# Optimization experiments

Measured on AMD Instinct MI355X. Metric: run time of the kernel, lower is better.

Reference implementation:

```python
import jax, jax.numpy as jnp
import numpy as np

B, T = 32, 64
C, H, W = 1, 32, 32
A, E, D, S, HID = 2, 64, 128, 32, 128
K, STRIDE, PAD = 4, 2, 1
FEAT = 64 * 4 * 4  # conv stack output: 64 channels at 4x4


def _lin(x, w, b):
    return x @ w.T + b


def _conv(x, w, b):
    y = jax.lax.conv_general_dilated(x, w, (STRIDE, STRIDE), [(PAD, PAD)] * 2,
                                     dimension_numbers=('NCHW', 'OIHW', 'NCHW'))
    return y + b[None, :, None, None]


def _deconv(x, w, b):
    # torch ConvTranspose2d(w: (in_c,out_c,k,k), stride=2, pad=1) as dilated conv
    w_ = jnp.flip(w, (2, 3)).transpose(1, 0, 2, 3)
    p = K - 1 - PAD
    y = jax.lax.conv_general_dilated(x, w_, (1, 1), [(p, p)] * 2,
                                     lhs_dilation=(STRIDE, STRIDE),
                                     dimension_numbers=('NCHW', 'OIHW', 'NCHW'))
    return y + b[None, :, None, None]


def _mlp(x, w1, b1, w2, b2, w3, b3):
    h = jax.nn.elu(_lin(x, w1, b1))
    h = jax.nn.elu(_lin(h, w2, b2))
    out = _lin(h, w3, b3)
    return out[..., :S], jnp.clip(out[..., S:], -5.0, 2.0)


def _gru(x, h, wih, whh, bih, bhh):
    # torch nn.GRUCell semantics
    gi = x @ wih.T + bih
    gh = h @ whh.T + bhh
    ir, iz, inn = jnp.split(gi, 3, -1)
    hr, hz, hn = jnp.split(gh, 3, -1)
    r = jax.nn.sigmoid(ir + hr)
    u = jax.nn.sigmoid(iz + hz)
    n = jnp.tanh(inn + r * hn)
    return (1.0 - u) * n + u * h


def setup_inputs():
    keys = iter(jax.random.split(jax.random.key(0), 64))

    def p(shape, fan):
        return jax.random.normal(next(keys), shape, jnp.float32) / np.sqrt(fan)

    return dict(
        obs=jax.random.normal(next(keys), (B, T, C, H, W), jnp.float32),
        actions=jax.random.normal(next(keys), (B, T, A), jnp.float32),
        noise=jax.random.normal(next(keys), (T, B, S), jnp.float32),
        enc_w1=p((32, C, K, K), C * K * K), enc_b1=jnp.zeros(32),
        enc_w2=p((64, 32, K, K), 32 * K * K), enc_b2=jnp.zeros(64),
        enc_w3=p((64, 64, K, K), 64 * K * K), enc_b3=jnp.zeros(64),
        enc_pw=p((E, FEAT), FEAT), enc_pb=jnp.zeros(E),
        dec_pw=p((FEAT, D + S), D + S), dec_pb=jnp.zeros(FEAT),
        dec_w1=p((64, 64, K, K), 64 * K * K), dec_b1=jnp.zeros(64),
        dec_w2=p((64, 32, K, K), 64 * K * K), dec_b2=jnp.zeros(32),
        dec_w3=p((32, C, K, K), 32 * K * K), dec_b3=jnp.zeros(C),
        gru_wih=p((3 * D, S + A), D), gru_whh=p((3 * D, D), D),
        gru_bih=jnp.zeros(3 * D), gru_bhh=jnp.zeros(3 * D),
        pri_w1=p((HID, D + A), D + A), pri_b1=jnp.zeros(HID),
        pri_w2=p((HID, HID), HID), pri_b2=jnp.zeros(HID),
        pri_w3=p((2 * S, HID), HID), pri_b3=jnp.zeros(2 * S),
        pos_w1=p((HID, D + E), D + E), pos_b1=jnp.zeros(HID),
        pos_w2=p((HID, HID), HID), pos_b2=jnp.zeros(HID),
        pos_w3=p((2 * S, HID), HID), pos_b3=jnp.zeros(2 * S),
    )


def reference(obs, actions, noise, enc_w1, enc_b1, enc_w2, enc_b2, enc_w3, enc_b3,
              enc_pw, enc_pb, dec_pw, dec_pb, dec_w1, dec_b1, dec_w2, dec_b2,
              dec_w3, dec_b3, gru_wih, gru_whh, gru_bih, gru_bhh,
              pri_w1, pri_b1, pri_w2, pri_b2, pri_w3, pri_b3,
              pos_w1, pos_b1, pos_w2, pos_b2, pos_w3, pos_b3):
    Bq, Tq = obs.shape[:2]
    # --- CNN encoder over all frames at once ---
    x = obs.reshape(Bq * Tq, C, H, W)
    x = jax.nn.relu(_conv(x, enc_w1, enc_b1))
    x = jax.nn.relu(_conv(x, enc_w2, enc_b2))
    x = jax.nn.relu(_conv(x, enc_w3, enc_b3))
    embed = _lin(x.reshape(Bq * Tq, -1), enc_pw, enc_pb).reshape(Bq, Tq, E)

    # --- sequential RSSM core (use_posterior=True path) ---
    def step(h, inp):
        a, e_t, eps = inp
        pm, pls = _mlp(jnp.concatenate([h, e_t], -1),
                       pos_w1, pos_b1, pos_w2, pos_b2, pos_w3, pos_b3)
        z = pm + jnp.exp(pls) * eps
        prm, prls = _mlp(jnp.concatenate([h, a], -1),
                         pri_w1, pri_b1, pri_w2, pri_b2, pri_w3, pri_b3)
        h_new = _gru(jnp.concatenate([z, a], -1), h, gru_wih, gru_whh, gru_bih, gru_bhh)
        return h_new, (z, prm, prls, pm, pls, h)  # h = pre-update (used for decode)

    h0 = jnp.zeros((Bq, D), obs.dtype)
    h_final, (zs, prm, prls, pm, pls, hs) = jax.lax.scan(
        step, h0, (actions.swapaxes(0, 1), embed.swapaxes(0, 1), noise))

    # --- batched decode of all (h_t, z_t); same math as per-step decode ---
    hz = jnp.concatenate([hs, zs], -1).reshape(Tq * Bq, D + S)
    y = _lin(hz, dec_pw, dec_pb).reshape(Tq * Bq, 64, 4, 4)
    y = jax.nn.relu(_deconv(y, dec_w1, dec_b1))
    y = jax.nn.relu(_deconv(y, dec_w2, dec_b2))
    y = jax.nn.sigmoid(_deconv(y, dec_w3, dec_b3))
    recons = y.reshape(Tq, Bq, C, H, W).swapaxes(0, 1)

    tb = lambda t: t.swapaxes(0, 1)  # (T,B,.) -> (B,T,.)
    return (recons, tb(zs), tb(prm), tb(prls), tb(pm), tb(pls), h_final)
```

## Files before the change

kernel.cpp:

```cpp
#include <hip/hip_runtime.h>
#include <math.h>

#define NB 32
#define NT 64
#define NF 2048

#define OUT_ZS    2097152
#define OUT_PRM   (OUT_ZS + 65536)
#define OUT_PRLS  (OUT_PRM + 65536)
#define OUT_PM    (OUT_PRLS + 65536)
#define OUT_PLS   (OUT_PM + 65536)
#define OUT_HF    (OUT_PLS + 65536)

#define WS_HS    27394048
#define WS_ENCT  27656192
#define WS_DECT  27721728
#define WS_WP1H  27885568
#define WS_WP2   27893760
#define WS_WP3   27901952
#define WS_WWHH  27906048
#define WS_WIHZ  27930624
#define WS_QW1T  27936768
#define WS_QW2T  27953408
#define WS_QW3T  27969792
#define WS_PW1T  27977984
#define WS_WIHT  28002560
#define WS_WC2   16777216
#define WS_WC3   (WS_WC2 + 16384)
#define WS_WD1   (WS_WC3 + 32768)
#define WS_WD2   (WS_WD1 + 32768)
#define WS_POSL1E 25165824
#define WS_GIA    (WS_POSL1E + 262144)

typedef __attribute__((ext_vector_type(8))) short short8;
typedef __attribute__((ext_vector_type(4))) float floatx4;
typedef _Float16 __attribute__((ext_vector_type(2))) half2v;
union U4S8 { uint4 u; short8 s; };
__device__ __forceinline__ short8 u2s(uint4 u) { U4S8 x; x.u = u; return x.s; }
__device__ __forceinline__ float eluf(float a) { return (a > 0.f) ? a : expm1f(a); }
__device__ __forceinline__ float sigm(float a) { return 1.f / (1.f + expf(-a)); }
__device__ __forceinline__ unsigned short f2bf(float f) {
  unsigned int u = __float_as_uint(f);
  u += 0x7fffu + ((u >> 16) & 1u);
  return (unsigned short)(u >> 16);
}
__device__ __forceinline__ unsigned short f2h(float f) {
  _Float16 h = (_Float16)f;
  return __builtin_bit_cast(unsigned short, h);
}
union UH2 { unsigned int u; half2v h; };
__device__ __forceinline__ half2v u2h(unsigned int u) { UH2 x; x.u = u; return x.h; }

__device__ __forceinline__ float fdot2w(half2v a, half2v b, float c) {
#if __has_builtin(__builtin_amdgcn_fdot2)
  return __builtin_amdgcn_fdot2(a, b, c, false);
#else
  return fmaf((float)a[0], (float)b[0], fmaf((float)a[1], (float)b[1], c));
#endif
}

union U4H2 { uint4 u; half2v h[4]; };
__device__ __forceinline__ void dot8h(uint4 w, uint4 x,
                                      float& a0, float& a1, float& a2, float& a3) {
  U4H2 W; W.u = w;
  U4H2 X; X.u = x;
  a0 = fdot2w(W.h[0], X.h[0], a0);
  a1 = fdot2w(W.h[1], X.h[1], a1);
  a2 = fdot2w(W.h[2], X.h[2], a2);
  a3 = fdot2w(W.h[3], X.h[3], a3);
}

struct PP { const float* src; void* dst; int n; int mode; int A; int B; };
struct PPAll { PP m[16]; };

__global__ __launch_bounds__(256) void k_prep(PPAll a) {
  PP p = a.m[blockIdx.y];
  for (int i = blockIdx.x * 256 + threadIdx.x; i < p.n; i += gridDim.x * 256) {
    if (p.mode == 10) {
      const int r = i / p.B, c = i - r * p.B;
      ((float*)p.dst)[c * p.A + r] = p.src[i];
    } else {
      float v;
      if (p.mode == 0) v = p.src[i];
      else if (p.mode == 1) v = p.src[(i >> 7) * 192 + (i & 127)];
      else if (p.mode == 2) v = p.src[(i >> 5) * 34 + (i & 31)];
      else if (p.mode == 5) {
        const int kq = i >> 12, o = (i >> 2) & 1023, kl = (i >> 1) & 1, h = i & 1;
        v = p.src[o * 160 + kq * 4 + kl * 2 + h];
      } else {
        const int ab = p.A * p.B;
        const int t = i / ab, rem = i - t * ab;
        const int oc = rem / p.B, ic = rem - oc * p.B;
        v = (p.mode == 3) ? p.src[(oc * p.B + ic) * 16 + t]
                          : p.src[(ic * p.A + oc) * 16 + t];
      }
      ((unsigned short*)p.dst)[i] = (p.mode <= 2 || p.mode == 5) ? f2h(v) : f2bf(v);
    }
  }
}

__global__ __launch_bounds__(256, 2) void k_enc(
    const float* __restrict__ obs, const float* __restrict__ act,
    const float* __restrict__ w1, const float* __restrict__ b1,
    const unsigned short* __restrict__ wc2, const float* __restrict__ b2,
    const unsigned short* __restrict__ wc3, const float* __restrict__ b3,
    const float* __restrict__ encT, const float* __restrict__ encb,
    const float* __restrict__ pw1T, const float* __restrict__ pb1,
    const float* __restrict__ wihT, const float* __restrict__ bih,
    float* __restrict__ posl1e, float* __restrict__ gia) {
  const int f = blockIdx.x, tid = threadIdx.x;
  const int w = tid >> 6, l = tid & 63, q = l >> 4, n = l & 15;
  __shared__ float sIn1[32 * 33];
  __shared__ float sW1[512];
  __shared__ float sB1[32];
  __shared__ __align__(16) unsigned short sIn2[18 * 18 * 40];
  __shared__ __align__(16) unsigned short sIn3[10 * 10 * 72];
  __shared__ __align__(16) float sXe[1024];
  __shared__ float sP[256];
  __shared__ float sE[64];
  __shared__ float sA2[2];

  {
    const float* in = obs + (size_t)f * 1024;
    for (int i = tid; i < 1024; i += 256) sIn1[(i >> 5) * 33 + (i & 31)] = in[i];
    for (int i = tid; i < 512; i += 256) sW1[i] = w1[i];
    if (tid < 32) sB1[tid] = b1[tid];
    if (tid < 2) sA2[tid] = act[(size_t)f * 2 + tid];
    unsigned int* z2 = (unsigned int*)sIn2;
    for (int i = tid; i < 18 * 18 * 40 / 2; i += 256) z2[i] = 0u;
    unsigned int* z3 = (unsigned int*)sIn3;
    for (int i = tid; i < 10 * 10 * 72 / 2; i += 256) z3[i] = 0u;
  }
  __syncthreads();
  for (int r = tid; r < 512; r += 256) {
    const int oc = r >> 4, oy = r & 15;
    float acc[16];
    const float bv = sB1[oc];
#pragma unroll
    for (int j = 0; j < 16; j++) acc[j] = bv;
#pragma unroll
    for (int ky = 0; ky < 4; ky++) {
      const int iy = 2 * oy + ky - 1;
      if (iy < 0 || iy >= 32) continue;
#pragma unroll
      for (int kx = 0; kx < 4; kx++) {
        const float wv = sW1[oc * 16 + ky * 4 + kx];
#pragma unroll
        for (int j = 0; j < 16; j++) {
          const int ix = 2 * j + kx - 1;
          if (ix >= 0 && ix < 32) acc[j] += wv * sIn1[iy * 33 + ix];
        }
      }
    }
#pragma unroll
    for (int j = 0; j < 16; j++)
      sIn2[((oy + 1) * 18 + (j + 1)) * 40 + oc] = f2bf(fmaxf(acc[j], 0.f));
  }
  __syncthreads();
  {
    int base[4];
#pragma unroll
    for (int nt = 0; nt < 4; nt++) {
      const int px = nt * 16 + n, oy = px >> 3, ox = px & 7;
      base[nt] = ((2 * oy + 1) * 18 + (2 * ox + 1)) * 40 + q * 8;
    }
    floatx4 acc[4];
#pragma unroll
    for (int nt = 0; nt < 4; nt++) acc[nt] = (floatx4){0.f, 0.f, 0.f, 0.f};
    uint4 af[16];
#pragma unroll
    for (int t = 0; t < 16; t++)
      af[t] = *reinterpret_cast<const uint4*>(wc2 + (size_t)(t * 64 + w * 16 + n) * 32 + q * 8);
#pragma unroll
    for (int t = 0; t < 16; t++) {
      const int toff = ((t / 4 - 1) * 18 + (t % 4 - 1)) * 40;
#pragma unroll
      for (int nt = 0; nt < 4; nt++) {
        uint4 bf = *reinterpret_cast<const uint4*>(&sIn2[base[nt] + toff]);
        acc[nt] = __builtin_amdgcn_mfma_f32_16x16x32_bf16(u2s(af[t]), u2s(bf), acc[nt], 0, 0, 0);
      }
    }
    float b4[4];
#pragma unroll
    for (int r = 0; r < 4; r++) b4[r] = b2[w * 16 + q * 4 + r];
    __syncthreads();
#pragma unroll
    for (int nt = 0; nt < 4; nt++) {
      const int px = nt * 16 + n, oy = px >> 3, ox = px & 7;
#pragma unroll
      for (int r = 0; r < 4; r++)
        sIn3[((oy + 1) * 10 + (ox + 1)) * 72 + (w * 16 + q * 4 + r)] =
            f2bf(fmaxf(acc[nt][r] + b4[r], 0.f));
    }
  }
  __syncthreads();
  {
    const int oy = n >> 2, ox = n & 3;
    const int ibase = ((2 * oy + 1) * 10 + (2 * ox + 1)) * 72 + q * 8;
    floatx4 acc = (floatx4){0.f, 0.f, 0.f, 0.f};
    for (int ks = 0; ks < 2; ks++) {
      uint4 af[16];
#pragma unroll
      for (int t = 0; t < 16; t++)
        af[t] = *reinterpret_cast<const uint4*>(
            wc3 + (size_t)(t * 64 + w * 16 + n) * 64 + ks * 32 + q * 8);
#pragma unroll
      for (int t = 0; t < 16; t++) {
        const int toff = ((t / 4 - 1) * 10 + (t % 4 - 1)) * 72 + ks * 32;
        uint4 bf = *reinterpret_cast<const uint4*>(&sIn3[ibase + toff]);
        acc = __builtin_amdgcn_mfma_f32_16x16x32_bf16(u2s(af[t]), u2s(bf), acc, 0, 0, 0);
      }
    }
#pragma unroll
    for (int r = 0; r < 4; r++) {
      const int ch = w * 16 + q * 4 + r;
      sXe[ch * 16 + n] = fmaxf(acc[r] + b3[ch], 0.f);
    }
  }
  __syncthreads();
  {
    const int o = tid & 63, s = tid >> 6;
    float acc = 0.f;
    const int k0 = s * 256;
    for (int k = k0; k < k0 + 256; k++) acc += encT[k * 64 + o] * sXe[k];
    sP[tid] = acc;
  }
  __syncthreads();
  if (tid < 64)
    sE[tid] = sP[tid] + sP[tid + 64] + sP[tid + 128] + sP[tid + 192] + encb[tid];
  __syncthreads();
  if (tid < 128) {
    float a = pb1[tid];
    for (int k = 0; k < 64; k++) a += pw1T[(128 + k) * 128 + tid] * sE[k];
    posl1e[(size_t)f * 128 + tid] = a;
  } else {
#pragma unroll
    for (int jj = 0; jj < 3; jj++) {
      const int j = (tid - 128) + jj * 128;
      gia[(size_t)f * 384 + j] =
          bih[j] + wihT[32 * 384 + j] * sA2[0] + wihT[33 * 384 + j] * sA2[1];
    }
  }
}

__global__ __launch_bounds__(512, 2) void k_rssm4(
    const float* __restrict__ posl1e, const float* __restrict__ gia,
    const float* __restrict__ noise,
    const unsigned short* __restrict__ wp1h, const unsigned short* __restrict__ wp2,
    const unsigned short* __restrict__ wp3, const unsigned short* __restrict__ wwhh,
    const unsigned short* __restrict__ wihz,
    const float* __restrict__ pb2, const float* __restrict__ pb3,
    const float* __restrict__ bhh,
    float* __restrict__ hs, float* __restrict__ out) {
  const int b = blockIdx.x, tid = threadIdx.x;
  __shared__ __align__(16) _Float16 sHh[128];
  __shared__ __align__(16) _Float16 sL1h[128];
  __shared__ __align__(16) _Float16 sL2h[128];
  __shared__ __align__(16) _Float16 sZh[32];
  __shared__ float sGh[384];

  uint4 wA[16];
  {
    const unsigned short* rowA =
        (tid < 128) ? (wp1h + tid * 128) : (wwhh + (size_t)(tid - 128) * 128);
#pragma unroll
    for (int i = 0; i < 16; i++) wA[i] = reinterpret_cast<const uint4*>(rowA)[i];
  }
  uint4 wB[4];
  {
    const unsigned short* rowB = wp2 + (tid >> 2) * 128 + (tid & 3) * 32;
#pragma unroll
    for (int i = 0; i < 4; i++) wB[i] = reinterpret_cast<const uint4*>(rowB)[i];
  }
  uint4 wC[2];
  {
    const int r = tid >> 3;
    const int o = (r >> 1) + ((r & 1) << 5);
    const unsigned short* rowC = wp3 + o * 128 + (tid & 7) * 16;
#pragma unroll
    for (int i = 0; i < 2; i++) wC[i] = reinterpret_cast<const uint4*>(rowC)[i];
  }
  uint4 wD[3][4];
  if (tid < 128) {
#pragma unroll
    for (int j = 0; j < 3; j++) {
      const unsigned short* rowD = wihz + (size_t)(tid + 128 * j) * 32;
#pragma unroll
      for (int i = 0; i < 4; i++) wD[j][i] = reinterpret_cast<const uint4*>(rowD)[i];
    }
  }
  const bool zlane = (tid & 15) == 0;
  const int jz = tid >> 4;
  const float bhhR = (tid >= 128) ? bhh[tid - 128] : 0.f;
  const float pb2R = pb2[tid >> 2];
  const float pb3mR = zlane ? pb3[jz] : 0.f;
  const float pb3sR = zlane ? pb3[jz + 32] : 0.f;

  float h_reg = 0.f;
  float pl1R = 0.f, gaR0 = 0.f, gaR1 = 0.f, gaR2 = 0.f, epsR = 0.f;
  if (tid < 128) {
    pl1R = posl1e[(size_t)(b * 64) * 128 + tid];
    const size_t gb = (size_t)(b * 64) * 384 + tid;
    gaR0 = gia[gb];
    gaR1 = gia[gb + 128];
    gaR2 = gia[gb + 256];
    sHh[tid] = (_Float16)0.f;
    hs[(size_t)b * 128 + tid] = 0.f;
  }
  if (zlane) epsR = noise[(size_t)b * 32 + jz];
  __syncthreads();

  for (int t = 0; t < 64; ++t) {
    const int tn = (t < 63) ? t + 1 : 63;
    float pl1N = 0.f, gaN0 = 0.f, gaN1 = 0.f, gaN2 = 0.f, epsN = 0.f;
    if (tid < 128) {
      pl1N = posl1e[(size_t)(b * 64 + tn) * 128 + tid];
      const size_t gb = (size_t)(b * 64 + tn) * 384 + tid;
      gaN0 = gia[gb];
      gaN1 = gia[gb + 128];
      gaN2 = gia[gb + 256];
    }
    if (zlane) epsN = noise[(size_t)(tn * 32 + b) * 32 + jz];

    {
      float a0 = 0.f, a1 = 0.f, a2 = 0.f, a3 = 0.f;
      const uint4* xs = reinterpret_cast<const uint4*>(sHh);
#pragma unroll
      for (int g = 0; g < 16; g++) dot8h(wA[g], xs[g], a0, a1, a2, a3);
      const float a = (a0 + a1) + (a2 + a3);
      if (tid < 128) sL1h[tid] = (_Float16)eluf(a + pl1R);
      else sGh[tid - 128] = a + bhhR;
    }
    __syncthreads();
    {
      float a0 = 0.f, a1 = 0.f, a2 = 0.f, a3 = 0.f;
      const uint4* xs = reinterpret_cast<const uint4*>(sL1h) + (tid & 3) * 4;
#pragma unroll
      for (int i = 0; i < 4; i++) dot8h(wB[i], xs[i], a0, a1, a2, a3);
      float p = (a0 + a1) + (a2 + a3);
      p += __shfl_xor(p, 1);
      p += __shfl_xor(p, 2);
      if ((tid & 3) == 0) sL2h[tid >> 2] = (_Float16)eluf(p + pb2R);
    }
    __syncthreads();
    {
      float a0 = 0.f, a1 = 0.f, a2 = 0.f, a3 = 0.f;
      const uint4* xs = reinterpret_cast<const uint4*>(sL2h) + (tid & 7) * 2;
      dot8h(wC[0], xs[0], a0, a1, a2, a3);
      dot8h(wC[1], xs[1], a0, a1, a2, a3);
      float p = (a0 + a1) + (a2 + a3);
      p += __shfl_xor(p, 1);
      p += __shfl_xor(p, 2);
      p += __shfl_xor(p, 4);
      const float pq = __shfl_xor(p, 8);
      if (zlane) {
        const float pm = p + pb3mR;
        float pls = pq + pb3sR;
        pls = fminf(fmaxf(pls, -5.f), 2.f);
        const float z = pm + expf(pls) * epsR;
        sZh[jz] = (_Float16)z;
        const int o = (b * 64 + t) * 32 + jz;
        out[OUT_ZS + o] = z;
        out[OUT_PM + o] = pm;
        out[OUT_PLS + o] = pls;
      }
    }
    __syncthreads();
    if (tid < 128) {
      float r0 = 0.f, r1 = 0.f, r2 = 0.f, r3 = 0.f;
      float u0 = 0.f, u1 = 0.f, u2 = 0.f, u3 = 0.f;
      float m0 = 0.f, m1 = 0.f, m2 = 0.f, m3 = 0.f;
      const uint4* xs = reinterpret_cast<const uint4*>(sZh);
#pragma unroll
      for (int i = 0; i < 4; i++) {
        const uint4 xv = xs[i];
        dot8h(wD[0][i], xv, r0, r1, r2, r3);
        dot8h(wD[1][i], xv, u0, u1, u2, u3);
        dot8h(wD[2][i], xv, m0, m1, m2, m3);
      }
      const float gr = gaR0 + ((r0 + r1) + (r2 + r3));
      const float gu = gaR1 + ((u0 + u1) + (u2 + u3));
      const float gn = gaR2 + ((m0 + m1) + (m2 + m3));
      const float r = sigm(gr + sGh[tid]);
      const float u = sigm(gu + sGh[128 + tid]);
      const float n = tanhf(gn + r * sGh[256 + tid]);
      const float hn = (1.f - u) * n + u * h_reg;
      h_reg = hn;
      sHh[tid] = (_Float16)hn;
      if (t < 63) hs[(size_t)((t + 1) * 32 + b) * 128 + tid] = hn;
    }
    pl1R = pl1N;
    gaR0 = gaN0;
    gaR1 = gaN1;
    gaR2 = gaN2;
    epsR = epsN;
    __syncthreads();
  }
  if (tid < 128) out[OUT_HF + b * 128 + tid] = h_reg;
}

__global__ __launch_bounds__(128) void k_pri(const float* __restrict__ hs,
    const float* __restrict__ act,
    const float* __restrict__ qw1T, const float* __restrict__ qb1,
    const float* __restrict__ qw2T, const float* __restrict__ qb2,
    const float* __restrict__ qw3T, const float* __restrict__ qb3,
    float* __restrict__ out) {
  __shared__ float sV[128], sW[128];
  __shared__ float sA2[2];
  const int f = blockIdx.x, tid = threadIdx.x;
  const int t = f >> 5, b = f & 31;
  sV[tid] = hs[(size_t)f * 128 + tid];
  if (tid < 2) sA2[tid] = act[(size_t)(b * 64 + t) * 2 + tid];
  __syncthreads();
  {
    float a = qb1[tid];
    for (int k = 0; k < 128; k++) a += qw1T[k * 128 + tid] * sV[k];
    a += qw1T[128 * 128 + tid] * sA2[0] + qw1T[129 * 128 + tid] * sA2[1];
    sW[tid] = eluf(a);
  }
  __syncthreads();
  {
    float a = qb2[tid];
    for (int k = 0; k < 128; k++) a += qw2T[k * 128 + tid] * sW[k];
    sV[tid] = eluf(a);
  }
  __syncthreads();
  if (tid < 64) {
    float a = qb3[tid];
    for (int k = 0; k < 128; k++) a += qw3T[k * 64 + tid] * sV[k];
    const int o = (b * 64 + t) * 32;
    if (tid < 32) out[OUT_PRM + o + tid] = a;
    else out[OUT_PRLS + o + tid - 32] = fminf(fmaxf(a, -5.f), 2.f);
  }
}

#define D3_ROW 580
#define D3_PX  36
__global__ __launch_bounds__(256, 4) void k_dec(
    const float* __restrict__ hs, const float* __restrict__ zs,
    const unsigned short* __restrict__ decTh, const float* __restrict__ decb,
    const unsigned short* __restrict__ wd1, const float* __restrict__ db1,
    const unsigned short* __restrict__ wd2, const float* __restrict__ db2,
    const float* __restrict__ w3, const float* __restrict__ b3,
    float* __restrict__ out) {
  const int f = blockIdx.x, tid = threadIdx.x;
  const int w = tid >> 6, l = tid & 63, q = l >> 4, n = l & 15;
  const int t = f >> 5, b = f & 31;
  __shared__ __align__(16) _Float16 sXh[160];
  __shared__ __align__(16) unsigned short sInD1[6 * 6 * 72];
  __shared__ __align__(16) unsigned short sInD2[10 * 10 * 72];
  __shared__ __align__(16) _Float16 sInD3h[16 * D3_ROW];
  __shared__ __align__(16) _Float16 sW3h[16 * 32];

  if (tid < 128) sXh[tid] = (_Float16)hs[(size_t)f * 128 + tid];
  else if (tid < 160) sXh[tid] = (_Float16)zs[(size_t)(b * 64 + t) * 32 + (tid - 128)];
  {
    unsigned int* z1 = (unsigned int*)sInD1;
    for (int i = tid; i < 6 * 6 * 72 / 2; i += 256) z1[i] = 0u;
    unsigned int* z2 = (unsigned int*)sInD2;
    for (int i = tid; i < 10 * 10 * 72 / 2; i += 256) z2[i] = 0u;
    for (int s = tid; s < 512; s += 256) {
      const int tap = s >> 5, icc = s & 31;
      sW3h[s] = (_Float16)w3[icc * 16 + tap];
    }
  }
  __syncthreads();
  {
    float acA[4] = {0.f, 0.f, 0.f, 0.f};
    float acB[4] = {0.f, 0.f, 0.f, 0.f};
    const uint2* dT = reinterpret_cast<const uint2*>(decTh);
    const unsigned int* xh = reinterpret_cast<const unsigned int*>(sXh);
#pragma unroll 2
    for (int kq = 0; kq < 40; kq++) {
      const half2v x0 = u2h(xh[2 * kq]);
      const half2v x1 = u2h(xh[2 * kq + 1]);
#pragma unroll
      for (int i = 0; i < 4; i++) {
        const uint2 wv = dT[kq * 1024 + i * 256 + tid];
        acA[i] = fdot2w(u2h(wv.x), x0, acA[i]);
        acB[i] = fdot2w(u2h(wv.y), x1, acB[i]);
      }
    }
#pragma unroll
    for (int i = 0; i < 4; i++) {
      const int o = i * 256 + tid, c = o >> 4, px = o & 15;
      const int Y = px >> 2, X = px & 3;
      sInD1[((Y + 1) * 6 + (X + 1)) * 72 + c] = f2bf(acA[i] + acB[i] + decb[o]);
    }
  }
  __syncthreads();
  {
    const int Y = n >> 2, X = n & 3;
    const int ibase = ((Y + 1) * 6 + (X + 1)) * 72 + q * 8;
    float b4[4];
#pragma unroll
    for (int r = 0; r < 4; r++) b4[r] = db1[w * 16 + q * 4 + r];
#pragma unroll
    for (int c = 0; c < 4; c++) {
      const int cy = c >> 1, cx = c & 1;
      floatx4 acc = (floatx4){0.f, 0.f, 0.f, 0.f};
      for (int ks = 0; ks < 2; ks++) {
        uint4 af[4];
#pragma unroll
        for (int tt = 0; tt < 4; tt++) {
          const int t2 = tt >> 1, t3 = tt & 1;
          const int ky = ((cy + 1) & 1) + 2 * t2, kx = ((cx + 1) & 1) + 2 * t3;
          af[tt] = *reinterpret_cast<const uint4*>(
              wd1 + (size_t)((ky * 4 + kx) * 64 + w * 16 + n) * 64 + ks * 32 + q * 8);
        }
#pragma unroll
        for (int tt = 0; tt < 4; tt++) {
          const int t2 = tt >> 1, t3 = tt & 1;
          const int toff = ((cy - t2) * 6 + (cx - t3)) * 72 + ks * 32;
          uint4 bf = *reinterpret_cast<const uint4*>(&sInD1[ibase + toff]);
          acc = __builtin_amdgcn_mfma_f32_16x16x32_bf16(u2s(af[tt]), u2s(bf), acc, 0, 0, 0);
        }
      }
      const int oy = 2 * Y + cy, ox = 2 * X + cx;
#pragma unroll
      for (int r = 0; r < 4; r++)
        sInD2[((oy + 1) * 10 + (ox + 1)) * 72 + (w * 16 + q * 4 + r)] =
            f2bf(fmaxf(acc[r] + b4[r], 0.f));
    }
  }
  __syncthreads();
  {
    const int px = w * 16 + n;
    const int Y = px >> 3, X = px & 7;
    const int ibase = ((Y + 1) * 10 + (X + 1)) * 72 + q * 8;
    float b4[2][4];
#pragma unroll
    for (int mi = 0; mi < 2; mi++)
#pragma unroll
      for (int r = 0; r < 4; r++) b4[mi][r] = db2[mi * 16 + q * 4 + r];
#pragma unroll
    for (int c = 0; c < 4; c++) {
      const int cy = c >> 1, cx = c & 1;
      floatx4 acc[2];
      acc[0] = (floatx4){0.f, 0.f, 0.f, 0.f};
      acc[1] = (floatx4){0.f, 0.f, 0.f, 0.f};
      for (int ks = 0; ks < 2; ks++) {
        uint4 af[2][4];
#pragma unroll
        for (int mi = 0; mi < 2; mi++)
#pragma unroll
          for (int tt = 0; tt < 4; tt++) {
            const int t2 = tt >> 1, t3 = tt & 1;
            const int ky = ((cy + 1) & 1) + 2 * t2, kx = ((cx + 1) & 1) + 2 * t3;
            af[mi][tt] = *reinterpret_cast<const uint4*>(
                wd2 + (size_t)((ky * 4 + kx) * 32 + mi * 16 + n) * 64 + ks * 32 + q * 8);
          }
#pragma unroll
        for (int tt = 0; tt < 4; tt++) {
          const int t2 = tt >> 1, t3 = tt & 1;
          const int toff = ((cy - t2) * 10 + (cx - t3)) * 72 + ks * 32;
          uint4 bf = *reinterpret_cast<const uint4*>(&sInD2[ibase + toff]);
#pragma unroll
          for (int mi = 0; mi < 2; mi++)
            acc[mi] = __builtin_amdgcn_mfma_f32_16x16x32_bf16(u2s(af[mi][tt]), u2s(bf),
                                                              acc[mi], 0, 0, 0);
        }
      }
      const int oy = 2 * Y + cy, ox = 2 * X + cx;
#pragma unroll
      for (int mi = 0; mi < 2; mi++) {
        const unsigned int lo =
            (unsigned int)f2h(fmaxf(acc[mi][0] + b4[mi][0], 0.f)) |
            ((unsigned int)f2h(fmaxf(acc[mi][1] + b4[mi][1], 0.f)) << 16);
        const unsigned int hi =
            (unsigned int)f2h(fmaxf(acc[mi][2] + b4[mi][2], 0.f)) |
            ((unsigned int)f2h(fmaxf(acc[mi][3] + b4[mi][3], 0.f)) << 16);
        *reinterpret_cast<uint2*>(&sInD3h[oy * D3_ROW + ox * D3_PX + mi * 16 + q * 4]) =
            make_uint2(lo, hi);
      }
    }
  }
  __syncthreads();
  {
    const int oy = tid >> 3;
    const int rem2 = tid & 7;
    const int cpar = rem2 >> 2, qq = rem2 & 3;
    const int py = (oy + 1) & 1, pc = (cpar + 1) & 1;
    const int ixb0 = (cpar + 1 - pc) >> 1;
    const int xlo = ixb0 - 1 + qq * 4;
    float acc[4] = {0.f, 0.f, 0.f, 0.f};
    const float bv = b3[0];
#pragma unroll
    for (int u2 = 0; u2 < 2; u2++) {
      const int ky = py + 2 * u2;
      const int iy = (oy + 1 - ky) >> 1;
      if (iy < 0 || iy >= 16) continue;
      const _Float16* rowp = &sInD3h[iy * D3_ROW];
      const uint2* wAp = reinterpret_cast<const uint2*>(&sW3h[(ky * 4 + pc) * 32]);
      const uint2* wBp = reinterpret_cast<const uint2*>(&sW3h[(ky * 4 + pc + 2) * 32]);
#pragma unroll
      for (int kb = 0; kb < 8; kb++) {
        uint2 xv[5];
#pragma unroll
        for (int x = 0; x < 5; x++) {
          const int ix = xlo + x;
          xv[x] = (ix >= 0 && ix < 16)
              ? *reinterpret_cast<const uint2*>(&rowp[ix * D3_PX + kb * 4])
              : make_uint2(0u, 0u);
        }
        const uint2 wa = wAp[kb], wb = wBp[kb];
#pragma unroll
        for (int j = 0; j < 4; j++) {
          acc[j] = fdot2w(u2h(wa.x), u2h(xv[j + 1].x), acc[j]);
          acc[j] = fdot2w(u2h(wa.y), u2h(xv[j + 1].y), acc[j]);
          acc[j] = fdot2w(u2h(wb.x), u2h(xv[j].x), acc[j]);
          acc[j] = fdot2w(u2h(wb.y), u2h(xv[j].y), acc[j]);
        }
      }
    }
    const int fo = b * 64 + t;
    float* yf = out + (size_t)fo * 1024;
#pragma unroll
    for (int j = 0; j < 4; j++)
      yf[oy * 32 + (cpar + 2 * (qq * 4 + j))] = 1.f / (1.f + expf(-(acc[j] + bv)));
  }
}

extern "C" void kernel_launch(void* const* d_in, const int* in_sizes, int n_in,
                              void* d_out, int out_size, void* d_ws, size_t ws_size,
                              hipStream_t stream) {
  const float* obs = (const float*)d_in[0];
  const float* actions = (const float*)d_in[1];
  const float* noise = (const float*)d_in[2];
  const float* enc_w1 = (const float*)d_in[3];
  const float* enc_b1 = (const float*)d_in[4];
  const float* enc_w2 = (const float*)d_in[5];
  const float* enc_b2 = (const float*)d_in[6];
  const float* enc_w3 = (const float*)d_in[7];
  const float* enc_b3 = (const float*)d_in[8];
  const float* enc_pw = (const float*)d_in[9];
  const float* enc_pb = (const float*)d_in[10];
  const float* dec_pw = (const float*)d_in[11];
  const float* dec_pb = (const float*)d_in[12];
  const float* dec_w1 = (const float*)d_in[13];
  const float* dec_b1 = (const float*)d_in[14];
  const float* dec_w2 = (const float*)d_in[15];
  const float* dec_b2 = (const float*)d_in[16];
  const float* dec_w3 = (const float*)d_in[17];
  const float* dec_b3 = (const float*)d_in[18];
  const float* gru_wih = (const float*)d_in[19];
  const float* gru_whh = (const float*)d_in[20];
  const float* gru_bih = (const float*)d_in[21];
  const float* gru_bhh = (const float*)d_in[22];
  const float* pri_w1 = (const float*)d_in[23];
  const float* pri_b1 = (const float*)d_in[24];
  const float* pri_w2 = (const float*)d_in[25];
  const float* pri_b2 = (const float*)d_in[26];
  const float* pri_w3 = (const float*)d_in[27];
  const float* pri_b3 = (const float*)d_in[28];
  const float* pos_w1 = (const float*)d_in[29];
  const float* pos_b1 = (const float*)d_in[30];
  const float* pos_w2 = (const float*)d_in[31];
  const float* pos_b2 = (const float*)d_in[32];
  const float* pos_w3 = (const float*)d_in[33];
  const float* pos_b3 = (const float*)d_in[34];

  float* out = (float*)d_out;
  float* ws = (float*)d_ws;
  float* HS = ws + WS_HS;
  float* POSL1E = ws + WS_POSL1E;
  float* GIA = ws + WS_GIA;
  unsigned short* WP1H = (unsigned short*)(ws + WS_WP1H);
  unsigned short* WP2 = (unsigned short*)(ws + WS_WP2);
  unsigned short* WP3 = (unsigned short*)(ws + WS_WP3);
  unsigned short* WWHH = (unsigned short*)(ws + WS_WWHH);
  unsigned short* WIHZ = (unsigned short*)(ws + WS_WIHZ);
  unsigned short* WC2 = (unsigned short*)(ws + WS_WC2);
  unsigned short* WC3 = (unsigned short*)(ws + WS_WC3);
  unsigned short* WD1 = (unsigned short*)(ws + WS_WD1);
  unsigned short* WD2 = (unsigned short*)(ws + WS_WD2);
  unsigned short* DECTH = (unsigned short*)(ws + WS_DECT);

  PPAll pp;
  pp.m[0]  = {enc_pw, ws + WS_ENCT, 64 * 1024, 10, 64, 1024};
  pp.m[1]  = {dec_pw, DECTH, 160 * 1024, 5, 0, 0};
  pp.m[2]  = {pri_w1, ws + WS_QW1T, 128 * 130, 10, 128, 130};
  pp.m[3]  = {pri_w2, ws + WS_QW2T, 128 * 128, 10, 128, 128};
  pp.m[4]  = {pri_w3, ws + WS_QW3T, 64 * 128, 10, 64, 128};
  pp.m[5]  = {pos_w1, ws + WS_PW1T, 128 * 192, 10, 128, 192};
  pp.m[6]  = {gru_wih, ws + WS_WIHT, 384 * 34, 10, 384, 34};
  pp.m[7]  = {pos_w1, WP1H, 128 * 128, 1, 0, 0};
  pp.m[8]  = {pos_w2, WP2, 128 * 128, 0, 0, 0};
  pp.m[9]  = {pos_w3, WP3, 64 * 128, 0, 0, 0};
  pp.m[10] = {gru_whh, WWHH, 384 * 128, 0, 0, 0};
  pp.m[11] = {gru_wih, WIHZ, 384 * 32, 2, 0, 0};
  pp.m[12] = {enc_w2, WC2, 16 * 64 * 32, 3, 64, 32};
  pp.m[13] = {enc_w3, WC3, 16 * 64 * 64, 3, 64, 64};
  pp.m[14] = {dec_w1, WD1, 16 * 64 * 64, 4, 64, 64};
  pp.m[15] = {dec_w2, WD2, 16 * 32 * 64, 4, 32, 64};
  hipLaunchKernelGGL(k_prep, dim3(32, 16), dim3(256), 0, stream, pp);

  k_enc<<<NF, 256, 0, stream>>>(obs, actions, enc_w1, enc_b1, WC2, enc_b2,
                                WC3, enc_b3, ws + WS_ENCT, enc_pb,
                                ws + WS_PW1T, pos_b1, ws + WS_WIHT, gru_bih,
                                POSL1E, GIA);

  k_rssm4<<<NB, 512, 0, stream>>>(POSL1E, GIA, noise, WP1H, WP2, WP3, WWHH, WIHZ,
                                  pos_b2, pos_b3, gru_bhh, HS, out);
  k_pri<<<NF, 128, 0, stream>>>(HS, actions, ws + WS_QW1T, pri_b1,
                                ws + WS_QW2T, pri_b2, ws + WS_QW3T, pri_b3, out);

  k_dec<<<NF, 256, 0, stream>>>(HS, out + OUT_ZS, DECTH, dec_pb,
                                WD1, dec_b1, WD2, dec_b2, dec_w3, dec_b3, out);
}
```

Before: 474.5 us.

## Batch decoder projection and prior MLP as MFMA GEMMs over 16-frame tiles

Moves the decoder's 160->1024 linear projection out of the per-frame decode kernel into a separate MFMA GEMM kernel that writes bf16 activations to workspace. The prior MLP, previously a scalar fp32 per-frame kernel, becomes an MFMA kernel handling 16 frames per block. Weight prep now emits row-major fp16 layouts, with the 130-wide prior input zero-padded to 160. The aim is to cut the redundant per-frame weight reads and scalar FMAs, at the cost of one extra launch, a workspace round trip and fp16 weights and activations in the prior MLP.

```diff
diff --git a/kernel.cpp b/kernel.cpp
--- a/kernel.cpp
+++ b/kernel.cpp
@@ -14,29 +14,33 @@
 
 #define WS_HS    27394048
 #define WS_ENCT  27656192
-#define WS_DECT  27721728
 #define WS_WP1H  27885568
 #define WS_WP2   27893760
 #define WS_WP3   27901952
 #define WS_WWHH  27906048
 #define WS_WIHZ  27930624
-#define WS_QW1T  27936768
-#define WS_QW2T  27953408
-#define WS_QW3T  27969792
 #define WS_PW1T  27977984
 #define WS_WIHT  28002560
 #define WS_WC2   16777216
 #define WS_WC3   (WS_WC2 + 16384)
 #define WS_WD1   (WS_WC3 + 32768)
 #define WS_WD2   (WS_WD1 + 32768)
+#define WS_DLIN  16908288
+#define WS_DECWF 17960960
+#define WS_QW1F  18045952
+#define WS_QW2F  18057216
+#define WS_QW3F  18066432
 #define WS_POSL1E 25165824
 #define WS_GIA    (WS_POSL1E + 262144)
 
 typedef __attribute__((ext_vector_type(8))) short short8;
 typedef __attribute__((ext_vector_type(4))) float floatx4;
 typedef _Float16 __attribute__((ext_vector_type(2))) half2v;
+typedef _Float16 __attribute__((ext_vector_type(8))) half8;
 union U4S8 { uint4 u; short8 s; };
 __device__ __forceinline__ short8 u2s(uint4 u) { U4S8 x; x.u = u; return x.s; }
+union U4HH { uint4 u; half8 h; };
+__device__ __forceinline__ half8 u2hh(uint4 u) { U4HH x; x.u = u; return x.h; }
 __device__ __forceinline__ float eluf(float a) { return (a > 0.f) ? a : expm1f(a); }
 __device__ __forceinline__ float sigm(float a) { return 1.f / (1.f + expf(-a)); }
 __device__ __forceinline__ unsigned short f2bf(float f) {
@@ -47,6 +51,9 @@
 __device__ __forceinline__ unsigned short f2h(float f) {
   _Float16 h = (_Float16)f;
   return __builtin_bit_cast(unsigned short, h);
+}
+__device__ __forceinline__ unsigned int pack2h(float a, float b) {
+  return (unsigned int)f2h(a) | ((unsigned int)f2h(b) << 16);
 }
 union UH2 { unsigned int u; half2v h; };
 __device__ __forceinline__ half2v u2h(unsigned int u) { UH2 x; x.u = u; return x.h; }
@@ -84,9 +91,9 @@
       if (p.mode == 0) v = p.src[i];
       else if (p.mode == 1) v = p.src[(i >> 7) * 192 + (i & 127)];
       else if (p.mode == 2) v = p.src[(i >> 5) * 34 + (i & 31)];
-      else if (p.mode == 5) {
-        const int kq = i >> 12, o = (i >> 2) & 1023, kl = (i >> 1) & 1, h = i & 1;
-        v = p.src[o * 160 + kq * 4 + kl * 2 + h];
+      else if (p.mode == 6) {
+        const int o = i / 160, k = i - o * 160;
+        v = (k < 130) ? p.src[o * 130 + k] : 0.f;
       } else {
         const int ab = p.A * p.B;
         const int t = i / ab, rem = i - t * ab;
@@ -94,7 +101,7 @@
         v = (p.mode == 3) ? p.src[(oc * p.B + ic) * 16 + t]
                           : p.src[(ic * p.A + oc) * 16 + t];
       }
-      ((unsigned short*)p.dst)[i] = (p.mode <= 2 || p.mode == 5) ? f2h(v) : f2bf(v);
+      ((unsigned short*)p.dst)[i] = (p.mode <= 2 || p.mode == 6) ? f2h(v) : f2bf(v);
     }
   }
 }
@@ -399,46 +406,121 @@
   if (tid < 128) out[OUT_HF + b * 128 + tid] = h_reg;
 }
 
-__global__ __launch_bounds__(128) void k_pri(const float* __restrict__ hs,
-    const float* __restrict__ act,
-    const float* __restrict__ qw1T, const float* __restrict__ qb1,
-    const float* __restrict__ qw2T, const float* __restrict__ qb2,
-    const float* __restrict__ qw3T, const float* __restrict__ qb3,
+__global__ __launch_bounds__(256) void k_declin(
+    const float* __restrict__ hs, const float* __restrict__ zs,
+    const unsigned short* __restrict__ decwf, const float* __restrict__ decb,
+    unsigned short* __restrict__ dlin) {
+  const int tid = threadIdx.x;
+  const int otile = blockIdx.x;
+  const int fBase = blockIdx.y * 16;
+  const int w = tid >> 6, l = tid & 63, q = l >> 4, n = l & 15;
+  __shared__ __align__(16) _Float16 sB[16][168];
+  for (int i = tid; i < 2560; i += 256) {
+    const int fr = i / 160, k = i - fr * 160;
+    const int f = fBase + fr;
+    float v;
+    if (k < 128) v = hs[(size_t)f * 128 + k];
+    else v = zs[(size_t)((f & 31) * 64 + (f >> 5)) * 32 + (k - 128)];
+    sB[fr][k] = (_Float16)v;
+  }
+  __syncthreads();
+  const int oB = otile * 64 + w * 16;
+  floatx4 acc = (floatx4){0.f, 0.f, 0.f, 0.f};
+#pragma unroll
+  for (int ks = 0; ks < 5; ks++) {
+    uint4 a = *reinterpret_cast<const uint4*>(&decwf[(size_t)(oB + n) * 160 + ks * 32 + q * 8]);
+    uint4 bb = *reinterpret_cast<const uint4*>(&sB[n][ks * 32 + q * 8]);
+    acc = __builtin_amdgcn_mfma_f32_16x16x32_f16(u2hh(a), u2hh(bb), acc, 0, 0, 0);
+  }
+  const int o0 = oB + q * 4;
+  const int f = fBase + n;
+  const unsigned int lo = (unsigned int)f2bf(acc[0] + decb[o0]) |
+                          ((unsigned int)f2bf(acc[1] + decb[o0 + 1]) << 16);
+  const unsigned int hi = (unsigned int)f2bf(acc[2] + decb[o0 + 2]) |
+                          ((unsigned int)f2bf(acc[3] + decb[o0 + 3]) << 16);
+  *reinterpret_cast<uint2*>(&dlin[(size_t)f * 1024 + o0]) = make_uint2(lo, hi);
+}
+
+__global__ __launch_bounds__(256) void k_pri_g(
+    const float* __restrict__ hs, const float* __restrict__ act,
+    const unsigned short* __restrict__ qw1f, const float* __restrict__ qb1,
+    const unsigned short* __restrict__ qw2f, const float* __restrict__ qb2,
+    const unsigned short* __restrict__ qw3f, const float* __restrict__ qb3,
     float* __restrict__ out) {
-  __shared__ float sV[128], sW[128];
-  __shared__ float sA2[2];
-  const int f = blockIdx.x, tid = threadIdx.x;
-  const int t = f >> 5, b = f & 31;
-  sV[tid] = hs[(size_t)f * 128 + tid];
-  if (tid < 2) sA2[tid] = act[(size_t)(b * 64 + t) * 2 + tid];
-  __syncthreads();
-  {
-    float a = qb1[tid];
-    for (int k = 0; k < 128; k++) a += qw1T[k * 128 + tid] * sV[k];
-    a += qw1T[128 * 128 + tid] * sA2[0] + qw1T[129 * 128 + tid] * sA2[1];
-    sW[tid] = eluf(a);
-  }
-  __syncthreads();
-  {
-    float a = qb2[tid];
-    for (int k = 0; k < 128; k++) a += qw2T[k * 128 + tid] * sW[k];
-    sV[tid] = eluf(a);
-  }
-  __syncthreads();
-  if (tid < 64) {
-    float a = qb3[tid];
-    for (int k = 0; k < 128; k++) a += qw3T[k * 64 + tid] * sV[k];
-    const int o = (b * 64 + t) * 32;
-    if (tid < 32) out[OUT_PRM + o + tid] = a;
-    else out[OUT_PRLS + o + tid - 32] = fminf(fmaxf(a, -5.f), 2.f);
+  const int tid = threadIdx.x;
+  const int fBase = blockIdx.x * 16;
+  const int w = tid >> 6, l = tid & 63, q = l >> 4, n = l & 15;
+  __shared__ __align__(16) _Float16 sB[16][168];
+  __shared__ __align__(16) _Float16 sB2[16][136];
+  for (int i = tid; i < 2560; i += 256) {
+    const int fr = i / 160, k = i - fr * 160;
+    const int f = fBase + fr;
+    float v = 0.f;
+    if (k < 128) v = hs[(size_t)f * 128 + k];
+    else if (k < 130) v = act[(size_t)((f & 31) * 64 + (f >> 5)) * 2 + (k - 128)];
+    sB[fr][k] = (_Float16)v;
+  }
+  __syncthreads();
+#pragma unroll
+  for (int g = 0; g < 2; g++) {
+    const int oB = g * 64 + w * 16;
+    floatx4 acc = (floatx4){0.f, 0.f, 0.f, 0.f};
+#pragma unroll
+    for (int ks = 0; ks < 5; ks++) {
+      uint4 a = *reinterpret_cast<const uint4*>(&qw1f[(oB + n) * 160 + ks * 32 + q * 8]);
+      uint4 bb = *reinterpret_cast<const uint4*>(&sB[n][ks * 32 + q * 8]);
+      acc = __builtin_amdgcn_mfma_f32_16x16x32_f16(u2hh(a), u2hh(bb), acc, 0, 0, 0);
+    }
+    const int o0 = oB + q * 4;
+    *reinterpret_cast<unsigned int*>(&sB2[n][o0]) =
+        pack2h(eluf(acc[0] + qb1[o0]), eluf(acc[1] + qb1[o0 + 1]));
+    *reinterpret_cast<unsigned int*>(&sB2[n][o0 + 2]) =
+        pack2h(eluf(acc[2] + qb1[o0 + 2]), eluf(acc[3] + qb1[o0 + 3]));
+  }
+  __syncthreads();
+#pragma unroll
+  for (int g = 0; g < 2; g++) {
+    const int oB = g * 64 + w * 16;
+    floatx4 acc = (floatx4){0.f, 0.f, 0.f, 0.f};
+#pragma unroll
+    for (int ks = 0; ks < 4; ks++) {
+      uint4 a = *reinterpret_cast<const uint4*>(&qw2f[(oB + n) * 128 + ks * 32 + q * 8]);
+      uint4 bb = *reinterpret_cast<const uint4*>(&sB2[n][ks * 32 + q * 8]);
+      acc = __builtin_amdgcn_mfma_f32_16x16x32_f16(u2hh(a), u2hh(bb), acc, 0, 0, 0);
+    }
+    const int o0 = oB + q * 4;
+    *reinterpret_cast<unsigned int*>(&sB[n][o0]) =
+        pack2h(eluf(acc[0] + qb2[o0]), eluf(acc[1] + qb2[o0 + 1]));
+    *reinterpret_cast<unsigned int*>(&sB[n][o0 + 2]) =
+        pack2h(eluf(acc[2] + qb2[o0 + 2]), eluf(acc[3] + qb2[o0 + 3]));
+  }
+  __syncthreads();
+  {
+    const int oB = w * 16;
+    floatx4 acc = (floatx4){0.f, 0.f, 0.f, 0.f};
+#pragma unroll
+    for (int ks = 0; ks < 4; ks++) {
+      uint4 a = *reinterpret_cast<const uint4*>(&qw3f[(oB + n) * 128 + ks * 32 + q * 8]);
+      uint4 bb = *reinterpret_cast<const uint4*>(&sB[n][ks * 32 + q * 8]);
+      acc = __builtin_amdgcn_mfma_f32_16x16x32_f16(u2hh(a), u2hh(bb), acc, 0, 0, 0);
+    }
+    const int o0 = oB + q * 4;
+    const int f = fBase + n;
+    const int ob = ((f & 31) * 64 + (f >> 5)) * 32;
+#pragma unroll
+    for (int r = 0; r < 4; r++) {
+      const int o = o0 + r;
+      const float v = acc[r] + qb3[o];
+      if (o < 32) out[OUT_PRM + ob + o] = v;
+      else out[OUT_PRLS + ob + o - 32] = fminf(fmaxf(v, -5.f), 2.f);
+    }
   }
 }
 
 #define D3_ROW 580
 #define D3_PX  36
 __global__ __launch_bounds__(256, 4) void k_dec(
-    const float* __restrict__ hs, const float* __restrict__ zs,
-    const unsigned short* __restrict__ decTh, const float* __restrict__ decb,
+    const unsigned short* __restrict__ dlin,
     const unsigned short* __restrict__ wd1, const float* __restrict__ db1,
     const unsigned short* __restrict__ wd2, const float* __restrict__ db2,
     const float* __restrict__ w3, const float* __restrict__ b3,
@@ -446,14 +528,12 @@
   const int f = blockIdx.x, tid = threadIdx.x;
   const int w = tid >> 6, l = tid & 63, q = l >> 4, n = l & 15;
   const int t = f >> 5, b = f & 31;
-  __shared__ __align__(16) _Float16 sXh[160];
   __shared__ __align__(16) unsigned short sInD1[6 * 6 * 72];
   __shared__ __align__(16) unsigned short sInD2[10 * 10 * 72];
   __shared__ __align__(16) _Float16 sInD3h[16 * D3_ROW];
   __shared__ __align__(16) _Float16 sW3h[16 * 32];
 
-  if (tid < 128) sXh[tid] = (_Float16)hs[(size_t)f * 128 + tid];
-  else if (tid < 160) sXh[tid] = (_Float16)zs[(size_t)(b * 64 + t) * 32 + (tid - 128)];
+  const uint2 dv = *reinterpret_cast<const uint2*>(dlin + (size_t)f * 1024 + tid * 4);
   {
     unsigned int* z1 = (unsigned int*)sInD1;
     for (int i = tid; i < 6 * 6 * 72 / 2; i += 256) z1[i] = 0u;
@@ -466,27 +546,13 @@
   }
   __syncthreads();
   {
-    float acA[4] = {0.f, 0.f, 0.f, 0.f};
-    float acB[4] = {0.f, 0.f, 0.f, 0.f};
-    const uint2* dT = reinterpret_cast<const uint2*>(decTh);
-    const unsigned int* xh = reinterpret_cast<const unsigned int*>(sXh);
-#pragma unroll 2
-    for (int kq = 0; kq < 40; kq++) {
-      const half2v x0 = u2h(xh[2 * kq]);
-      const half2v x1 = u2h(xh[2 * kq + 1]);
-#pragma unroll
-      for (int i = 0; i < 4; i++) {
-        const uint2 wv = dT[kq * 1024 + i * 256 + tid];
-        acA[i] = fdot2w(u2h(wv.x), x0, acA[i]);
-        acB[i] = fdot2w(u2h(wv.y), x1, acB[i]);
-      }
-    }
-#pragma unroll
-    for (int i = 0; i < 4; i++) {
-      const int o = i * 256 + tid, c = o >> 4, px = o & 15;
-      const int Y = px >> 2, X = px & 3;
-      sInD1[((Y + 1) * 6 + (X + 1)) * 72 + c] = f2bf(acA[i] + acB[i] + decb[o]);
-    }
+    const int o0 = tid * 4, c = o0 >> 4, px0 = o0 & 15;
+    const int Y = px0 >> 2;
+    const int base = ((Y + 1) * 6 + 1) * 72 + c;
+    sInD1[base] = (unsigned short)(dv.x & 0xffffu);
+    sInD1[base + 72] = (unsigned short)(dv.x >> 16);
+    sInD1[base + 144] = (unsigned short)(dv.y & 0xffffu);
+    sInD1[base + 216] = (unsigned short)(dv.y >> 16);
   }
   __syncthreads();
   {
@@ -674,14 +740,18 @@
   unsigned short* WC3 = (unsigned short*)(ws + WS_WC3);
   unsigned short* WD1 = (unsigned short*)(ws + WS_WD1);
   unsigned short* WD2 = (unsigned short*)(ws + WS_WD2);
-  unsigned short* DECTH = (unsigned short*)(ws + WS_DECT);
+  unsigned short* DLIN = (unsigned short*)(ws + WS_DLIN);
+  unsigned short* DECWF = (unsigned short*)(ws + WS_DECWF);
+  unsigned short* QW1F = (unsigned short*)(ws + WS_QW1F);
+  unsigned short* QW2F = (unsigned short*)(ws + WS_QW2F);
+  unsigned short* QW3F = (unsigned short*)(ws + WS_QW3F);
 
   PPAll pp;
   pp.m[0]  = {enc_pw, ws + WS_ENCT, 64 * 1024, 10, 64, 1024};
-  pp.m[1]  = {dec_pw, DECTH, 160 * 1024, 5, 0, 0};
-  pp.m[2]  = {pri_w1, ws + WS_QW1T, 128 * 130, 10, 128, 130};
-  pp.m[3]  = {pri_w2, ws + WS_QW2T, 128 * 128, 10, 128, 128};
-  pp.m[4]  = {pri_w3, ws + WS_QW3T, 64 * 128, 10, 64, 128};
+  pp.m[1]  = {dec_pw, DECWF, 1024 * 160, 0, 0, 0};
+  pp.m[2]  = {pri_w1, QW1F, 128 * 160, 6, 0, 0};
+  pp.m[3]  = {pri_w2, QW2F, 128 * 128, 0, 0, 0};
+  pp.m[4]  = {pri_w3, QW3F, 64 * 128, 0, 0, 0};
   pp.m[5]  = {pos_w1, ws + WS_PW1T, 128 * 192, 10, 128, 192};
   pp.m[6]  = {gru_wih, ws + WS_WIHT, 384 * 34, 10, 384, 34};
   pp.m[7]  = {pos_w1, WP1H, 128 * 128, 1, 0, 0};
@@ -702,9 +772,10 @@
 
   k_rssm4<<<NB, 512, 0, stream>>>(POSL1E, GIA, noise, WP1H, WP2, WP3, WWHH, WIHZ,
                                   pos_b2, pos_b3, gru_bhh, HS, out);
-  k_pri<<<NF, 128, 0, stream>>>(HS, actions, ws + WS_QW1T, pri_b1,
-                                ws + WS_QW2T, pri_b2, ws + WS_QW3T, pri_b3, out);
-
-  k_dec<<<NF, 256, 0, stream>>>(HS, out + OUT_ZS, DECTH, dec_pb,
-                                WD1, dec_b1, WD2, dec_b2, dec_w3, dec_b3, out);
-}
+
+  k_declin<<<dim3(16, 128), 256, 0, stream>>>(HS, out + OUT_ZS, DECWF, dec_pb, DLIN);
+  k_pri_g<<<128, 256, 0, stream>>>(HS, actions, QW1F, pri_b1,
+                                   QW2F, pri_b2, QW3F, pri_b3, out);
+
+  k_dec<<<NF, 256, 0, stream>>>(DLIN, WD1, dec_b1, WD2, dec_b2, dec_w3, dec_b3, out);
+}
```

After: 448.9 us. 5.4% less time.
